# Kernel optimization log

Measured on AMD Instinct MI355X. Metric: run time of the kernel, lower is better.

## Reference

```python
import math
import jax, jax.numpy as jnp
import numpy as np

T = 2048       # sequence_length
H = 2048       # hidden_size
NH = 32        # num_attention_heads
NKV = 8        # num_key_value_heads
HD = 64        # head_dim
SW = 128       # sliding_window
QM = NH // NKV # q_mult (GQA group size)
ROPE_THETA = 10000.0
EPS = 1e-5


def setup_inputs() -> dict:
    key = jax.random.key(0)
    k_x, k_s, k_qkv, k_out = jax.random.split(key, 4)
    x = jax.random.normal(k_x, (T, H), dtype=jnp.float32)
    scale = jnp.ones((H,), dtype=jnp.float32)
    sinks = jax.random.normal(k_s, (NH,), dtype=jnp.float32) * 0.02
    qkv_dim = HD * (NH + 2 * NKV)  # 3072
    qkv_kernel = jax.random.normal(k_qkv, (H, qkv_dim), dtype=jnp.float32) * (1.0 / math.sqrt(H))
    qkv_bias = jnp.zeros((qkv_dim,), dtype=jnp.float32)
    out_kernel = jax.random.normal(k_out, (H, H), dtype=jnp.float32) * (1.0 / math.sqrt(H))
    out_bias = jnp.zeros((H,), dtype=jnp.float32)
    # RoPE tables: [T, HD//2]
    half = HD // 2
    inv_freq = 1.0 / (ROPE_THETA ** (np.arange(half, dtype=np.float64) / half))
    ang = np.outer(np.arange(T, dtype=np.float64), inv_freq)
    cos_table = jnp.asarray(np.cos(ang), dtype=jnp.float32)
    sin_table = jnp.asarray(np.sin(ang), dtype=jnp.float32)
    # causal + sliding-window additive mask [T, T]
    qp = np.arange(T, dtype=np.int32)[:, None]
    kp = np.arange(T, dtype=np.int32)[None, :]
    m = np.where(kp > qp, -np.inf, 0.0) + np.where(qp - kp > SW, -np.inf, 0.0)
    mask = jnp.asarray(m, dtype=jnp.float32)
    return dict(x=x, scale=scale, sinks=sinks, qkv_kernel=qkv_kernel,
                qkv_bias=qkv_bias, out_kernel=out_kernel, out_bias=out_bias,
                cos_table=cos_table, sin_table=sin_table, mask=mask)


def _rmsnorm(x, scale):
    t = x.astype(jnp.float32)
    rms = jnp.sqrt(jnp.mean(t * t, axis=-1, keepdims=True) + EPS)
    return ((t / rms) * scale).astype(x.dtype)


def _rope(x, cos, sin):
    # x: [T, ..., HD]; split-half rotation as in the reference RotaryEmbedding
    shp = x.shape
    xr = x.reshape(shp[0], -1, HD)
    c = cos[:, None, :].astype(xr.dtype)
    s = sin[:, None, :].astype(xr.dtype)
    x1, x2 = jnp.split(xr, 2, axis=-1)
    y = jnp.concatenate([x1 * c - x2 * s, x2 * c + x1 * s], axis=-1)
    return y.reshape(shp)


def reference(x, scale, sinks, qkv_kernel, qkv_bias, out_kernel, out_bias,
              cos_table, sin_table, mask):
    normed = _rmsnorm(x, scale)
    qkv = normed @ qkv_kernel + qkv_bias                 # [T, 3072]
    q_end = NH * HD
    k_end = q_end + NKV * HD
    q = qkv[:, :q_end].reshape(T, NKV, QM, HD)           # [T, nkv, qm, hd]
    k = qkv[:, q_end:k_end].reshape(T, NKV, HD)          # [T, nkv, hd]
    v = qkv[:, k_end:].reshape(T, NKV, HD)               # [T, nkv, hd]
    q = _rope(q, cos_table, sin_table)
    k = _rope(k, cos_table, sin_table)
    sm_scale = 1.0 / math.sqrt(float(HD))
    # GQA attention without materializing repeated K/V
    logits = jnp.einsum('qnmd,knd->nmqk', q, k) * sm_scale  # [nkv, qm, T, T]
    logits = logits + mask[None, None, :, :]
    sink_col = jnp.broadcast_to(sinks.reshape(NKV, QM, 1, 1), (NKV, QM, T, 1))
    logits = jnp.concatenate([logits, sink_col], axis=-1)   # [nkv, qm, T, T+1]
    weights = jax.nn.softmax(logits, axis=-1)[..., :-1]     # drop sink column
    attn = jnp.einsum('nmqk,knd->qnmd', weights, v).reshape(T, NH * HD)
    projected = attn @ out_kernel + out_bias
    return x + projected
```

## Files before the change

### kernel.cpp

```cpp
#include <hip/hip_runtime.h>
#include <hip/hip_bf16.h>
#include <stdint.h>

typedef __bf16 bf16_t;
typedef __attribute__((ext_vector_type(8))) __bf16 bf16x8;
typedef __attribute__((ext_vector_type(4))) __bf16 bf16x4;
typedef __attribute__((ext_vector_type(4))) float f32x4;

static constexpr int T_SEQ = 2048;
static constexpr int HID   = 2048;
static constexpr int NHEAD = 32;
static constexpr int NKVH  = 8;
static constexpr int HDIM  = 64;
static constexpr int QKVD  = 3072;

__device__ inline f32x4 mfma16(bf16x8 a, bf16x8 b, f32x4 c) {
    return __builtin_amdgcn_mfma_f32_16x16x32_bf16(a, b, c, 0, 0, 0);
}

__device__ inline void load_lds16(const bf16_t* g, bf16_t* l) {
    __builtin_amdgcn_global_load_lds(
        (const __attribute__((address_space(1))) void*)g,
        (__attribute__((address_space(3))) void*)l, 16, 0, 0);
}

__global__ __launch_bounds__(256) void transpose_cast(const float* __restrict__ in,
                                                      bf16_t* __restrict__ out,
                                                      int K, int N) {
    __shared__ float tile[32][33];
    int tx = threadIdx.x & 31, ty = threadIdx.x >> 5;
    int bx = blockIdx.x, by = blockIdx.y;
#pragma unroll
    for (int i = 0; i < 4; ++i)
        tile[ty + 8*i][tx] = in[(size_t)(by*32 + ty + 8*i)*N + bx*32 + tx];
    __syncthreads();
#pragma unroll
    for (int i = 0; i < 4; ++i)
        out[(size_t)(bx*32 + ty + 8*i)*K + by*32 + tx] = (bf16_t)tile[tx][ty + 8*i];
}

__global__ __launch_bounds__(256) void rmsnorm_cast(const float* __restrict__ x,
                                                    const float* __restrict__ scale,
                                                    bf16_t* __restrict__ out) {
    int row = blockIdx.x;
    int tid = threadIdx.x;
    const float4* x4 = (const float4*)(x + (size_t)row * HID);
    const float4* s4 = (const float4*)scale;
    float4 v0 = x4[tid], v1 = x4[tid + 256];
    float ss = v0.x*v0.x + v0.y*v0.y + v0.z*v0.z + v0.w*v0.w
             + v1.x*v1.x + v1.y*v1.y + v1.z*v1.z + v1.w*v1.w;
#pragma unroll
    for (int off = 32; off > 0; off >>= 1) ss += __shfl_down(ss, off);
    __shared__ float wsum[4];
    if ((tid & 63) == 0) wsum[tid >> 6] = ss;
    __syncthreads();
    float total = wsum[0] + wsum[1] + wsum[2] + wsum[3];
    float inv = rsqrtf(total * (1.0f / HID) + 1e-5f);
    float4 sc0 = s4[tid], sc1 = s4[tid + 256];
    bf16_t* outr = out + (size_t)row * HID;
    bf16x4 o0, o1;
    o0.x = (bf16_t)(v0.x*inv*sc0.x); o0.y = (bf16_t)(v0.y*inv*sc0.y);
    o0.z = (bf16_t)(v0.z*inv*sc0.z); o0.w = (bf16_t)(v0.w*inv*sc0.w);
    o1.x = (bf16_t)(v1.x*inv*sc1.x); o1.y = (bf16_t)(v1.y*inv*sc1.y);
    o1.z = (bf16_t)(v1.z*inv*sc1.z); o1.w = (bf16_t)(v1.w*inv*sc1.w);
    *(bf16x4*)(outr + 4*tid)        = o0;
    *(bf16x4*)(outr + 1024 + 4*tid) = o1;
}

__global__ __launch_bounds__(256) void gemm_splitk(const bf16_t* __restrict__ A,
                                                   const bf16_t* __restrict__ Bt,
                                                   bf16_t* __restrict__ Cpart,
                                                   int M, int N, int K) {
    __shared__ __align__(16) bf16_t Asm[128 * 32];
    __shared__ __align__(16) bf16_t Bsm[128 * 32];
    const int tid = threadIdx.x;
    const int bm = blockIdx.y * 128, bn = blockIdx.x * 128;
    const int kh = K >> 1;
    const int kb = blockIdx.z * kh;
    const int lane = tid & 63, wave = tid >> 6;
    const int wm = (wave & 1) * 64, wn = (wave >> 1) * 64;
    const int lm = lane & 15, quad = lane >> 4;

    f32x4 acc[4][4];
#pragma unroll
    for (int i = 0; i < 4; ++i)
#pragma unroll
        for (int j = 0; j < 4; ++j) acc[i][j] = (f32x4){0.f, 0.f, 0.f, 0.f};

    const int cid0 = wave * 64 + lane;
    const int cid1 = cid0 + 256;
    const int r0 = cid0 >> 2, c0 = (cid0 & 3) ^ ((r0 >> 1) & 3);
    const int r1 = cid1 >> 2, c1 = (cid1 & 3) ^ ((r1 >> 1) & 3);
    const bf16_t* Ab = A  + (size_t)bm * K + kb;
    const bf16_t* Bb = Bt + (size_t)bn * K + kb;
    const size_t ga0 = (size_t)r0 * K + c0 * 8;
    const size_t ga1 = (size_t)r1 * K + c1 * 8;
    bf16_t* lds0 = &Asm[wave * 512];
    bf16_t* lds1 = &Asm[2048 + wave * 512];
    bf16_t* ldsB0 = &Bsm[wave * 512];
    bf16_t* ldsB1 = &Bsm[2048 + wave * 512];

    const int swz = (quad ^ ((lm >> 1) & 3)) * 8;

    for (int k0 = 0; k0 < kh; k0 += 32) {
        load_lds16(Ab + ga0 + k0, lds0);
        load_lds16(Ab + ga1 + k0, lds1);
        load_lds16(Bb + ga0 + k0, ldsB0);
        load_lds16(Bb + ga1 + k0, ldsB1);
        __syncthreads();
        bf16x8 af[4], bfr[4];
#pragma unroll
        for (int i = 0; i < 4; ++i)
            af[i]  = *(const bf16x8*)&Asm[(wm + i*16 + lm)*32 + swz];
#pragma unroll
        for (int j = 0; j < 4; ++j)
            bfr[j] = *(const bf16x8*)&Bsm[(wn + j*16 + lm)*32 + swz];
#pragma unroll
        for (int i = 0; i < 4; ++i)
#pragma unroll
            for (int j = 0; j < 4; ++j) acc[i][j] = mfma16(af[i], bfr[j], acc[i][j]);
        __syncthreads();
    }

    bf16_t* Cp = Cpart + (size_t)blockIdx.z * M * N;
#pragma unroll
    for (int i = 0; i < 4; ++i) {
        int gr = bm + wm + i*16 + quad*4;
#pragma unroll
        for (int j = 0; j < 4; ++j) {
            int gc = bn + wn + j*16 + lm;
#pragma unroll
            for (int r = 0; r < 4; ++r)
                Cp[(size_t)(gr + r)*N + gc] = (bf16_t)acc[i][j][r];
        }
    }
}

__global__ __launch_bounds__(256) void rope_split(const bf16_t* __restrict__ qp0,
                                                  const bf16_t* __restrict__ qp1,
                                                  const float* __restrict__ qbias,
                                                  const float* __restrict__ cost,
                                                  const float* __restrict__ sint,
                                                  bf16_t* __restrict__ Qb,
                                                  bf16_t* __restrict__ Kb,
                                                  bf16_t* __restrict__ Vb) {
    int t = blockIdx.x;
    const bf16_t* row0 = qp0 + (size_t)t * QKVD;
    const bf16_t* row1 = qp1 + (size_t)t * QKVD;
    const float* c = cost + (size_t)t * 32;
    const float* s = sint + (size_t)t * 32;
    for (int idx = threadIdx.x; idx < 1536; idx += 256) {
        int h = idx >> 5;
        int p = idx & 31;
        float x1 = (float)row0[h*64 + p]      + (float)row1[h*64 + p]      + qbias[h*64 + p];
        float x2 = (float)row0[h*64 + p + 32] + (float)row1[h*64 + p + 32] + qbias[h*64 + p + 32];
        float o1, o2;
        if (h < 40) { float cc = c[p], ssn = s[p]; o1 = x1*cc - x2*ssn; o2 = x2*cc + x1*ssn; }
        else        { o1 = x1; o2 = x2; }
        bf16_t b1 = (bf16_t)o1, b2 = (bf16_t)o2;
        if (h < 32) {
            bf16_t* q = Qb + ((size_t)t*NHEAD + h)*HDIM;
            q[p] = b1; q[p + 32] = b2;
        } else if (h < 40) {
            bf16_t* k = Kb + ((size_t)t*NKVH + (h - 32))*HDIM;
            k[p] = b1; k[p + 32] = b2;
        } else {
            bf16_t* v = Vb + ((size_t)t*NKVH + (h - 40))*HDIM;
            v[p] = b1; v[p + 32] = b2;
        }
    }
}

__global__ __launch_bounds__(256) void combine_out(const bf16_t* __restrict__ p0,
                                                   const bf16_t* __restrict__ p1,
                                                   const float* __restrict__ bias,
                                                   const float* __restrict__ x,
                                                   float* __restrict__ out) {
    const int n4 = T_SEQ * HID / 4;
    for (int i4 = blockIdx.x * 256 + threadIdx.x; i4 < n4; i4 += gridDim.x * 256) {
        bf16x4 a = *(const bf16x4*)(p0 + (size_t)i4 * 4);
        bf16x4 b = *(const bf16x4*)(p1 + (size_t)i4 * 4);
        float4 xv = *(const float4*)(x + (size_t)i4 * 4);
        int col4 = (i4 * 4) & (HID - 1);
        float4 bi = *(const float4*)(bias + col4);
        float4 o;
        o.x = (float)a.x + (float)b.x + bi.x + xv.x;
        o.y = (float)a.y + (float)b.y + bi.y + xv.y;
        o.z = (float)a.z + (float)b.z + bi.z + xv.z;
        o.w = (float)a.w + (float)b.w + bi.w + xv.w;
        *(float4*)(out + (size_t)i4 * 4) = o;
    }
}

__global__ __launch_bounds__(256) void attn_kernel(const bf16_t* __restrict__ Qb,
                                                   const bf16_t* __restrict__ Kb,
                                                   const bf16_t* __restrict__ Vb,
                                                   const float* __restrict__ sinks,
                                                   bf16_t* __restrict__ attnb) {
    __shared__ __align__(16) char smem[62464];
    bf16_t* Qs = (bf16_t*)smem;
    bf16_t* Ks = (bf16_t*)(smem + 9216);
    bf16_t* Vt = (bf16_t*)(smem + 36864);
    bf16_t* Ws = (bf16_t*)smem;

    const int tid = threadIdx.x;
    const int qt = blockIdx.x, h = blockIdx.y;
    const int qs = qt * 64;
    const int nkv = h >> 2;

#pragma unroll
    for (int it = 0; it < 2; ++it) {
        int cc = tid + it*256;
        int row = cc >> 3, off = (cc & 7) * 8;
        uint4 v = *(const uint4*)(Qb + ((size_t)(qs + row)*NHEAD + h)*HDIM + off);
        *(uint4*)&Qs[row*72 + off] = v;
    }
#pragma unroll
    for (int it = 0; it < 6; ++it) {
        int cc = tid + it*256;
        int j = cc >> 3, off = (cc & 7) * 8;
        int kg = qs - 128 + j;
        uint4 kv = {0, 0, 0, 0}, vv = {0, 0, 0, 0};
        if (kg >= 0) {
            kv = *(const uint4*)(Kb + ((size_t)kg*NKVH + nkv)*HDIM + off);
            vv = *(const uint4*)(Vb + ((size_t)kg*NKVH + nkv)*HDIM + off);
        }
        *(uint4*)&Ks[j*72 + off] = kv;
        union { uint4 u; bf16_t e[8]; } uv; uv.u = vv;
#pragma unroll
        for (int r = 0; r < 8; ++r) Vt[(off + r)*200 + j] = uv.e[r];
    }
    __syncthreads();

    const int lane = tid & 63, wave = tid >> 6;
    const int lm = lane & 15, quad = lane >> 4;
    const int w16 = wave * 16;

    f32x4 S[12];
#pragma unroll
    for (int jt = 0; jt < 12; ++jt) S[jt] = (f32x4){0.f, 0.f, 0.f, 0.f};
#pragma unroll
    for (int ks = 0; ks < 2; ++ks) {
        bf16x8 aq = *(const bf16x8*)&Qs[(w16 + lm)*72 + ks*32 + quad*8];
#pragma unroll
        for (int jt = 0; jt < 12; ++jt) {
            bf16x8 bk = *(const bf16x8*)&Ks[(jt*16 + lm)*72 + ks*32 + quad*8];
            S[jt] = mfma16(aq, bk, S[jt]);
        }
    }
    __syncthreads();

    const float sink = sinks[h];
#pragma unroll
    for (int reg = 0; reg < 4; ++reg) {
        const int qg = qs + w16 + quad*4 + reg;
        float mx = -1e30f;
#pragma unroll
        for (int jt = 0; jt < 12; ++jt) {
            int kg = qs - 128 + jt*16 + lm;
            float sv = S[jt][reg] * 0.125f;
            bool valid = (kg >= 0) && (kg <= qg) && (qg - kg <= 128);
            sv = valid ? sv : -1e30f;
            S[jt][reg] = sv;
            mx = fmaxf(mx, sv);
        }
#pragma unroll
        for (int off = 1; off < 16; off <<= 1) mx = fmaxf(mx, __shfl_xor(mx, off));
        float M = fmaxf(mx, sink);
        float sum = 0.f;
#pragma unroll
        for (int jt = 0; jt < 12; ++jt) {
            float e = __expf(S[jt][reg] - M);
            S[jt][reg] = e; sum += e;
        }
#pragma unroll
        for (int off = 1; off < 16; off <<= 1) sum += __shfl_xor(sum, off);
        float rden = 1.f / (sum + __expf(sink - M));
#pragma unroll
        for (int jt = 0; jt < 12; ++jt)
            Ws[(w16 + quad*4 + reg)*200 + jt*16 + lm] = (bf16_t)(S[jt][reg] * rden);
    }
    __syncthreads();

    f32x4 O[4];
#pragma unroll
    for (int nt = 0; nt < 4; ++nt) O[nt] = (f32x4){0.f, 0.f, 0.f, 0.f};
#pragma unroll
    for (int ks = 0; ks < 6; ++ks) {
        bf16x8 aw = *(const bf16x8*)&Ws[(w16 + lm)*200 + ks*32 + quad*8];
#pragma unroll
        for (int nt = 0; nt < 4; ++nt) {
            bf16x8 bv = *(const bf16x8*)&Vt[(nt*16 + lm)*200 + ks*32 + quad*8];
            O[nt] = mfma16(aw, bv, O[nt]);
        }
    }
#pragma unroll
    for (int nt = 0; nt < 4; ++nt)
#pragma unroll
        for (int reg = 0; reg < 4; ++reg)
            attnb[(size_t)(qs + w16 + quad*4 + reg)*HID + h*HDIM + nt*16 + lm] =
                (bf16_t)(O[nt][reg]);
}

extern "C" void kernel_launch(void* const* d_in, const int* in_sizes, int n_in,
                              void* d_out, int out_size, void* d_ws, size_t ws_size,
                              hipStream_t stream) {
    (void)in_sizes; (void)n_in; (void)out_size; (void)ws_size;
    const float* x          = (const float*)d_in[0];
    const float* scale      = (const float*)d_in[1];
    const float* sinks      = (const float*)d_in[2];
    const float* qkv_kernel = (const float*)d_in[3];
    const float* qkv_bias   = (const float*)d_in[4];
    const float* out_kernel = (const float*)d_in[5];
    const float* out_bias   = (const float*)d_in[6];
    const float* cos_t      = (const float*)d_in[7];
    const float* sin_t      = (const float*)d_in[8];
    float* out = (float*)d_out;

    char* ws = (char*)d_ws;
    const size_t MiB = 1048576;
    bf16_t* Wt_out = (bf16_t*)(ws);
    bf16_t* Wt_qkv = (bf16_t*)(ws + 8*MiB);
    bf16_t* attnb  = (bf16_t*)(ws + 8*MiB);
    bf16_t* normed = (bf16_t*)(ws + 20*MiB);
    bf16_t* qkvp   = (bf16_t*)(ws + 28*MiB);
    bf16_t* outp   = (bf16_t*)(ws + 28*MiB);
    bf16_t* Qb     = (bf16_t*)(ws + 52*MiB);
    bf16_t* Kb     = (bf16_t*)(ws + 60*MiB);
    bf16_t* Vb     = (bf16_t*)(ws + 62*MiB);

    transpose_cast<<<dim3(QKVD/32, HID/32), 256, 0, stream>>>(qkv_kernel, Wt_qkv, HID, QKVD);
    transpose_cast<<<dim3(HID/32,  HID/32), 256, 0, stream>>>(out_kernel, Wt_out, HID, HID);
    rmsnorm_cast<<<T_SEQ, 256, 0, stream>>>(x, scale, normed);
    gemm_splitk<<<dim3(QKVD/128, T_SEQ/128, 2), 256, 0, stream>>>(normed, Wt_qkv, qkvp,
                                                                  T_SEQ, QKVD, HID);
    rope_split<<<T_SEQ, 256, 0, stream>>>(qkvp, qkvp + (size_t)T_SEQ*QKVD, qkv_bias,
                                          cos_t, sin_t, Qb, Kb, Vb);
    attn_kernel<<<dim3(T_SEQ/64, NHEAD), 256, 0, stream>>>(Qb, Kb, Vb, sinks, attnb);
    gemm_splitk<<<dim3(HID/128, T_SEQ/128, 2), 256, 0, stream>>>(attnb, Wt_out, outp,
                                                                 T_SEQ, HID, HID);
    combine_out<<<2048, 256, 0, stream>>>(outp, outp + (size_t)T_SEQ*HID, out_bias, x, out);
}
```

Measured before the change: 235.0 us.

## Vectorize weight transpose and rope, read Q/K directly from global in attention

Merges the two weight transpose kernels into one launch using 64x64 tiles, float4 loads and 16-byte bf16 stores. Rewrites rope_split so each thread handles 8 contiguous elements with vector loads and stores. In attention, Q and K are now read straight from global memory into MFMA operands instead of being staged in LDS, and the V transpose writes paired elements. This cuts LDS use and one barrier, but adds uncoalesced global reads for K and a possible ordering hazard on the LDS buffers.

Measured after the change: 235.0 us. Within noise of the previous version (+0.0%).

```diff
diff --git a/kernel.cpp b/kernel.cpp
--- a/kernel.cpp
+++ b/kernel.cpp
@@ -24,19 +24,34 @@
         (__attribute__((address_space(3))) void*)l, 16, 0, 0);
 }
 
-__global__ __launch_bounds__(256) void transpose_cast(const float* __restrict__ in,
-                                                      bf16_t* __restrict__ out,
-                                                      int K, int N) {
-    __shared__ float tile[32][33];
-    int tx = threadIdx.x & 31, ty = threadIdx.x >> 5;
-    int bx = blockIdx.x, by = blockIdx.y;
-#pragma unroll
-    for (int i = 0; i < 4; ++i)
-        tile[ty + 8*i][tx] = in[(size_t)(by*32 + ty + 8*i)*N + bx*32 + tx];
+__global__ __launch_bounds__(256) void transpose_both(const float* __restrict__ Wq,
+                                                      const float* __restrict__ Wo,
+                                                      bf16_t* __restrict__ Tq,
+                                                      bf16_t* __restrict__ To) {
+    __shared__ float tile[64 * 65];
+    int b = blockIdx.x;
+    const float* in; bf16_t* out; int NN, KK, bx, by;
+    if (b < 1536) { in = Wq; out = Tq; NN = QKVD; KK = HID; bx = b % 48; by = b / 48; }
+    else { b -= 1536; in = Wo; out = To; NN = HID; KK = HID; bx = b % 32; by = b / 32; }
+    const int t = threadIdx.x;
+    const int c4 = (t & 15) * 4;
+#pragma unroll
+    for (int i = 0; i < 4; ++i) {
+        int r = (t >> 4) + i * 16;
+        float4 v = *(const float4*)(in + (size_t)(by*64 + r) * NN + bx*64 + c4);
+        tile[r*65 + c4 + 0] = v.x; tile[r*65 + c4 + 1] = v.y;
+        tile[r*65 + c4 + 2] = v.z; tile[r*65 + c4 + 3] = v.w;
+    }
     __syncthreads();
-#pragma unroll
-    for (int i = 0; i < 4; ++i)
-        out[(size_t)(bx*32 + ty + 8*i)*K + by*32 + tx] = (bf16_t)tile[tx][ty + 8*i];
+    const int kc = t & 7;
+#pragma unroll
+    for (int i = 0; i < 2; ++i) {
+        int n = (t >> 3) + i * 32;
+        bf16x8 o;
+#pragma unroll
+        for (int j = 0; j < 8; ++j) o[j] = (bf16_t)tile[(kc*8 + j)*65 + n];
+        *(bf16x8*)(out + (size_t)(bx*64 + n) * KK + by*64 + kc*8) = o;
+    }
 }
 
 __global__ __launch_bounds__(256) void rmsnorm_cast(const float* __restrict__ x,
@@ -136,7 +151,7 @@
     }
 }
 
-__global__ __launch_bounds__(256) void rope_split(const bf16_t* __restrict__ qp0,
+__global__ __launch_bounds__(192) void rope_split(const bf16_t* __restrict__ qp0,
                                                   const bf16_t* __restrict__ qp1,
                                                   const float* __restrict__ qbias,
                                                   const float* __restrict__ cost,
@@ -144,31 +159,41 @@
                                                   bf16_t* __restrict__ Qb,
                                                   bf16_t* __restrict__ Kb,
                                                   bf16_t* __restrict__ Vb) {
-    int t = blockIdx.x;
-    const bf16_t* row0 = qp0 + (size_t)t * QKVD;
-    const bf16_t* row1 = qp1 + (size_t)t * QKVD;
-    const float* c = cost + (size_t)t * 32;
-    const float* s = sint + (size_t)t * 32;
-    for (int idx = threadIdx.x; idx < 1536; idx += 256) {
-        int h = idx >> 5;
-        int p = idx & 31;
-        float x1 = (float)row0[h*64 + p]      + (float)row1[h*64 + p]      + qbias[h*64 + p];
-        float x2 = (float)row0[h*64 + p + 32] + (float)row1[h*64 + p + 32] + qbias[h*64 + p + 32];
-        float o1, o2;
-        if (h < 40) { float cc = c[p], ssn = s[p]; o1 = x1*cc - x2*ssn; o2 = x2*cc + x1*ssn; }
-        else        { o1 = x1; o2 = x2; }
-        bf16_t b1 = (bf16_t)o1, b2 = (bf16_t)o2;
-        if (h < 32) {
-            bf16_t* q = Qb + ((size_t)t*NHEAD + h)*HDIM;
-            q[p] = b1; q[p + 32] = b2;
-        } else if (h < 40) {
-            bf16_t* k = Kb + ((size_t)t*NKVH + (h - 32))*HDIM;
-            k[p] = b1; k[p + 32] = b2;
-        } else {
-            bf16_t* v = Vb + ((size_t)t*NKVH + (h - 40))*HDIM;
-            v[p] = b1; v[p + 32] = b2;
-        }
-    }
+    const int t = blockIdx.x;
+    const int hr = threadIdx.x >> 2, p0 = (threadIdx.x & 3) * 8;
+    const bf16_t* r0 = qp0 + (size_t)t * QKVD + hr * 64;
+    const bf16_t* r1 = qp1 + (size_t)t * QKVD + hr * 64;
+    bf16x8 a1 = *(const bf16x8*)(r0 + p0);
+    bf16x8 a2 = *(const bf16x8*)(r0 + p0 + 32);
+    bf16x8 b1 = *(const bf16x8*)(r1 + p0);
+    bf16x8 b2 = *(const bf16x8*)(r1 + p0 + 32);
+    const float* qb = qbias + hr * 64;
+    float x1[8], x2[8];
+#pragma unroll
+    for (int j = 0; j < 8; ++j) {
+        x1[j] = (float)a1[j] + (float)b1[j] + qb[p0 + j];
+        x2[j] = (float)a2[j] + (float)b2[j] + qb[p0 + j + 32];
+    }
+    bf16x8 w1, w2;
+    if (hr < 40) {
+        const float* c = cost + (size_t)t * 32 + p0;
+        const float* s = sint + (size_t)t * 32 + p0;
+#pragma unroll
+        for (int j = 0; j < 8; ++j) {
+            float cc = c[j], ss = s[j];
+            w1[j] = (bf16_t)(x1[j]*cc - x2[j]*ss);
+            w2[j] = (bf16_t)(x2[j]*cc + x1[j]*ss);
+        }
+    } else {
+#pragma unroll
+        for (int j = 0; j < 8; ++j) { w1[j] = (bf16_t)x1[j]; w2[j] = (bf16_t)x2[j]; }
+    }
+    bf16_t* dst;
+    if (hr < 32)      dst = Qb + ((size_t)t*NHEAD + hr)      * HDIM;
+    else if (hr < 40) dst = Kb + ((size_t)t*NKVH + (hr-32))  * HDIM;
+    else              dst = Vb + ((size_t)t*NKVH + (hr-40))  * HDIM;
+    *(bf16x8*)(dst + p0)      = w1;
+    *(bf16x8*)(dst + p0 + 32) = w2;
 }
 
 __global__ __launch_bounds__(256) void combine_out(const bf16_t* __restrict__ p0,
@@ -197,11 +222,8 @@
                                                    const bf16_t* __restrict__ Vb,
                                                    const float* __restrict__ sinks,
                                                    bf16_t* __restrict__ attnb) {
-    __shared__ __align__(16) char smem[62464];
-    bf16_t* Qs = (bf16_t*)smem;
-    bf16_t* Ks = (bf16_t*)(smem + 9216);
-    bf16_t* Vt = (bf16_t*)(smem + 36864);
-    bf16_t* Ws = (bf16_t*)smem;
+    __shared__ __align__(16) bf16_t Vt[64 * 200];
+    __shared__ __align__(16) bf16_t Ws[64 * 200];
 
     const int tid = threadIdx.x;
     const int qt = blockIdx.x, h = blockIdx.y;
@@ -209,28 +231,21 @@
     const int nkv = h >> 2;
 
 #pragma unroll
-    for (int it = 0; it < 2; ++it) {
-        int cc = tid + it*256;
-        int row = cc >> 3, off = (cc & 7) * 8;
-        uint4 v = *(const uint4*)(Qb + ((size_t)(qs + row)*NHEAD + h)*HDIM + off);
-        *(uint4*)&Qs[row*72 + off] = v;
-    }
-#pragma unroll
-    for (int it = 0; it < 6; ++it) {
-        int cc = tid + it*256;
-        int j = cc >> 3, off = (cc & 7) * 8;
-        int kg = qs - 128 + j;
-        uint4 kv = {0, 0, 0, 0}, vv = {0, 0, 0, 0};
-        if (kg >= 0) {
-            kv = *(const uint4*)(Kb + ((size_t)kg*NKVH + nkv)*HDIM + off);
-            vv = *(const uint4*)(Vb + ((size_t)kg*NKVH + nkv)*HDIM + off);
-        }
-        *(uint4*)&Ks[j*72 + off] = kv;
-        union { uint4 u; bf16_t e[8]; } uv; uv.u = vv;
-#pragma unroll
-        for (int r = 0; r < 8; ++r) Vt[(off + r)*200 + j] = uv.e[r];
-    }
-    __syncthreads();
+    for (int it = 0; it < 3; ++it) {
+        int pu = tid + it * 256;
+        int j = (pu >> 3) * 2, off = (pu & 7) * 8;
+        int kg0 = qs - 128 + j; if (kg0 < 0) kg0 = 0;
+        int kg1 = qs - 128 + j + 1; if (kg1 < 0) kg1 = 0;
+        union { uint4 u; bf16_t e[8]; } v0, v1;
+        v0.u = *(const uint4*)(Vb + ((size_t)kg0*NKVH + nkv)*HDIM + off);
+        v1.u = *(const uint4*)(Vb + ((size_t)kg1*NKVH + nkv)*HDIM + off);
+#pragma unroll
+        for (int r = 0; r < 8; ++r) {
+            union { uint u; bf16_t e[2]; } p;
+            p.e[0] = v0.e[r]; p.e[1] = v1.e[r];
+            *(uint*)&Vt[(off + r)*200 + j] = p.u;
+        }
+    }
 
     const int lane = tid & 63, wave = tid >> 6;
     const int lm = lane & 15, quad = lane >> 4;
@@ -239,16 +254,22 @@
     f32x4 S[12];
 #pragma unroll
     for (int jt = 0; jt < 12; ++jt) S[jt] = (f32x4){0.f, 0.f, 0.f, 0.f};
+    const bf16_t* Qrow = Qb + ((size_t)(qs + w16 + lm)*NHEAD + h)*HDIM + quad*8;
+    int krow[12];
+#pragma unroll
+    for (int jt = 0; jt < 12; ++jt) {
+        int kg = qs - 128 + jt*16 + lm;
+        krow[jt] = kg < 0 ? 0 : kg;
+    }
 #pragma unroll
     for (int ks = 0; ks < 2; ++ks) {
-        bf16x8 aq = *(const bf16x8*)&Qs[(w16 + lm)*72 + ks*32 + quad*8];
+        bf16x8 aq = *(const bf16x8*)(Qrow + ks*32);
 #pragma unroll
         for (int jt = 0; jt < 12; ++jt) {
-            bf16x8 bk = *(const bf16x8*)&Ks[(jt*16 + lm)*72 + ks*32 + quad*8];
+            bf16x8 bk = *(const bf16x8*)(Kb + ((size_t)krow[jt]*NKVH + nkv)*HDIM + ks*32 + quad*8);
             S[jt] = mfma16(aq, bk, S[jt]);
         }
     }
-    __syncthreads();
 
     const float sink = sinks[h];
 #pragma unroll
@@ -329,12 +350,11 @@
     bf16_t* Kb     = (bf16_t*)(ws + 60*MiB);
     bf16_t* Vb     = (bf16_t*)(ws + 62*MiB);
 
-    transpose_cast<<<dim3(QKVD/32, HID/32), 256, 0, stream>>>(qkv_kernel, Wt_qkv, HID, QKVD);
-    transpose_cast<<<dim3(HID/32,  HID/32), 256, 0, stream>>>(out_kernel, Wt_out, HID, HID);
+    transpose_both<<<2560, 256, 0, stream>>>(qkv_kernel, out_kernel, Wt_qkv, Wt_out);
     rmsnorm_cast<<<T_SEQ, 256, 0, stream>>>(x, scale, normed);
     gemm_splitk<<<dim3(QKVD/128, T_SEQ/128, 2), 256, 0, stream>>>(normed, Wt_qkv, qkvp,
                                                                   T_SEQ, QKVD, HID);
-    rope_split<<<T_SEQ, 256, 0, stream>>>(qkvp, qkvp + (size_t)T_SEQ*QKVD, qkv_bias,
+    rope_split<<<T_SEQ, 192, 0, stream>>>(qkvp, qkvp + (size_t)T_SEQ*QKVD, qkv_bias,
                                           cos_t, sin_t, Qb, Kb, Vb);
     attn_kernel<<<dim3(T_SEQ/64, NHEAD), 256, 0, stream>>>(Qb, Kb, Vb, sinks, attnb);
     gemm_splitk<<<dim3(HID/128, T_SEQ/128, 2), 256, 0, stream>>>(attnb, Wt_out, outp,
```
